# Performance work log

Measured on AMD Instinct MI355X. Metric: run time of the kernel, lower is better.

The kernel has to match this reference:

```python
import jax, jax.numpy as jnp
import numpy as np

D = 200; H = 4; DH = D // H
N_ETYPE = 38; N_NTYPE = 4
B = 256; L = 1024; E = B * L
NODES_PER_G = 200; N = B * NODES_PER_G


def _bn(x, g, b):
    # BatchNorm1d in training mode: batch stats over rows (biased variance, eps=1e-5)
    m = x.mean(axis=0)
    v = x.var(axis=0)
    return (x - m) * jax.lax.rsqrt(v + 1e-5) * g + b


def setup_inputs():
    key = jax.random.key(0)
    ks = jax.random.split(key, 24)
    f = lambda k, s: jax.random.normal(k, s, jnp.float32) * 0.02
    head = jax.random.randint(ks[0], (E,), 0, N)
    tail = (head + 1 + jax.random.randint(ks[1], (E,), 0, N - 1)) % N  # guaranteed no self-loops
    return {
        "x": jax.random.normal(ks[2], (N, D), jnp.float32),
        "node_feature_extra": jax.random.normal(ks[3], (N, D), jnp.float32),
        "sent_vec_r": jax.random.normal(ks[4], (B, D), jnp.float32),
        "We1": f(ks[5], (N_ETYPE + 1 + 2 * N_NTYPE, D)), "be1": jnp.zeros((D,), jnp.float32),
        "ge1": jnp.ones((D,), jnp.float32), "bte1": jnp.zeros((D,), jnp.float32),
        "We2": f(ks[6], (D, D)), "be2": jnp.zeros((D,), jnp.float32),
        "Wa1": f(ks[7], (2 * D, D)), "ba1": jnp.zeros((D,), jnp.float32),
        "ga1": jnp.ones((D,), jnp.float32), "bta1": jnp.zeros((D,), jnp.float32),
        "Wa2": f(ks[8], (D, D)), "ba2": jnp.zeros((D,), jnp.float32),
        "Watt": f(ks[9], (D, D)),
        "Wk": f(ks[10], (2 * D, D)), "bk": jnp.zeros((D,), jnp.float32),
        "Wm": f(ks[11], (2 * D, D)), "bm": jnp.zeros((D,), jnp.float32),
        "Wq": f(ks[12], (D, D)), "bq": jnp.zeros((D,), jnp.float32),
        "Wo1": f(ks[13], (D, D)), "bo1": jnp.zeros((D,), jnp.float32),
        "go1": jnp.ones((D,), jnp.float32), "bto1": jnp.zeros((D,), jnp.float32),
        "Wo2": f(ks[14], (D, D)), "bo2": jnp.zeros((D,), jnp.float32),
        "edge_index": jnp.stack([head, tail]),
        "edge_type": jax.random.randint(ks[15], (E,), 0, N_ETYPE),
        "node_type": jax.random.randint(ks[16], (N,), 0, N_NTYPE),
        "edges_per_graph": L,
    }


def reference(x, node_feature_extra, sent_vec_r, We1, be1, ge1, bte1, We2, be2,
              Wa1, ba1, ga1, bta1, Wa2, ba2, Watt, Wk, bk, Wm, bm, Wq, bq,
              Wo1, bo1, go1, bto1, Wo2, bo2,
              edge_index, edge_type, node_type, edges_per_graph):
    E_, N_ = edge_index.shape[1], x.shape[0]
    src, dst = edge_index[0], edge_index[1]
    x_head, x_tail = x[src], x[dst]
    x_fact = x_tail - x_head
    nt = N_ETYPE + 1
    # original does this segment-mean on detached CPU numpy -> no gradient path
    xf = jax.lax.stop_gradient(x_fact)
    sums = jax.ops.segment_sum(xf, edge_type, num_segments=nt)
    cnts = jax.ops.segment_sum(jnp.ones((E_,), x.dtype), edge_type, num_segments=nt)
    result = (sums / jnp.maximum(cnts, 1.0)[:, None])[edge_type]  # [E, D]
    # one-hot edge/node-type features for real edges + self edges
    edge_vec = jax.nn.one_hot(edge_type, nt, dtype=x.dtype)
    self_edge_vec = jnp.zeros((N_, nt), x.dtype).at[:, N_ETYPE].set(1.0)
    ht = jnp.concatenate([jax.nn.one_hot(node_type[src], N_NTYPE, dtype=x.dtype),
                          jax.nn.one_hot(node_type[dst], N_NTYPE, dtype=x.dtype)], 1)
    sh = jax.nn.one_hot(node_type, N_NTYPE, dtype=x.dtype)
    feat = jnp.concatenate([jnp.concatenate([edge_vec, ht], 1),
                            jnp.concatenate([self_edge_vec, sh, sh], 1)], 0)  # [E+N, 47]
    emb = jax.nn.relu(_bn(feat @ We1 + be1, ge1, bte1)) @ We2 + be2  # edge_encoder, [E+N, D]
    emb_e, emb_self = emb[:E_], emb[E_:]
    # edge_encoder_again on cat([emb_e, result]); split matmul avoids the [E,2D] concat
    h2 = _bn(emb_e @ Wa1[:D] + result @ Wa1[D:] + ba1, ga1, bta1)
    R = jax.nn.relu(h2) @ Wa2 + ba2  # [E, D]
    # per-graph attention: Q rows within a graph are identical (repeated sent_vec),
    # so the LxL softmax has identical rows -> compute one row per graph and broadcast.
    Bg = E_ // edges_per_graph
    Rg = R.reshape(Bg, edges_per_graph, D)
    q = sent_vec_r @ Watt  # [B, D]
    scores = jnp.einsum('bd,bld->bl', q, Rg) / jnp.sqrt(jnp.asarray(D, x.dtype))
    attn = jax.nn.softmax(scores, axis=1)
    upd = jnp.einsum('bl,bld->bd', attn, Rg)
    updated_R = jnp.broadcast_to(upd[:, None, :], Rg.shape).reshape(E_, D)
    edge_attr = jnp.concatenate([updated_R, emb_self], 0)
    # append self-loops (input edge_index has none, matching remove_self_loops)
    loop = jnp.arange(N_, dtype=src.dtype)
    src_all = jnp.concatenate([src, loop])
    dst_all = jnp.concatenate([dst, loop])
    x_i, x_j = x[dst_all], x[src_all]
    key_ = (x_i @ Wk[:D] + edge_attr @ Wk[D:] + bk).reshape(-1, H, DH)
    msg = (x_j @ Wm[:D] + edge_attr @ Wm[D:] + bm).reshape(-1, H, DH)
    qry = ((x_j @ Wq + bq) / jnp.sqrt(jnp.asarray(DH, x.dtype))).reshape(-1, H, DH)
    sc = (qry * key_).sum(-1)  # [E+N, H]
    # segment softmax grouped by source node (every segment non-empty due to self-loops)
    smax = jax.ops.segment_max(sc, src_all, num_segments=N_)
    ex = jnp.exp(sc - smax[src_all])
    den = jax.ops.segment_sum(ex, src_all, num_segments=N_)
    alpha = ex / den[src_all]
    cnt = jax.ops.segment_sum(jnp.ones((src_all.shape[0],), x.dtype), src_all, num_segments=N_)
    alpha = alpha * cnt[src_all][:, None]
    m = (msg * alpha[:, :, None]).reshape(-1, D)
    aggr = jax.ops.segment_sum(m, dst_all, num_segments=N_)  # scatter-add at targets
    return jax.nn.relu(_bn(aggr @ Wo1 + bo1, go1, bto1)) @ Wo2 + bo2
```

## Files before the change

kernel.cpp:

```cpp
#include <hip/hip_runtime.h>

#define D     200
#define H     4
#define DH    50
#define NE    38
#define NTY   4
#define NC    608
#define NCT   612
#define BG    256
#define LG    1024
#define EE    262144
#define NN    51200
#define EA    313344
#define NB    200

#define NTILES 13
#define KSTEPS 7
#define NMATS  8
#define SLICE_SHORTS 13312
#define NCHUNK 26
#define MROWS  128

typedef __attribute__((ext_vector_type(4))) float  f32x4;
typedef __attribute__((ext_vector_type(8))) short  bf16x8;

__device__ __forceinline__ short bf_hi(float f) {
    unsigned u = __float_as_uint(f);
    unsigned r = u + 0x7fffu + ((u >> 16) & 1u);
    return (short)(r >> 16);
}
__device__ __forceinline__ float bf_f(short s) {
    return __uint_as_float(((unsigned)(unsigned short)s) << 16);
}

__global__ __launch_bounds__(256) void k_hist(const int* __restrict__ ei, const int* __restrict__ et,
                                              const int* __restrict__ nt, int* outdeg, int* indeg,
                                              int* __restrict__ hcnt, float* coef) {
    __shared__ int loc[NC];
    int g = blockIdx.x, t = threadIdx.x;
    for (int i = t; i < NC; i += 256) loc[i] = 0;
    __syncthreads();
    #pragma unroll
    for (int j = 0; j < 4; j++) {
        int e = g * LG + j * 256 + t;
        int s = ei[e], d = ei[EE + e], tp = et[e];
        int c = tp * 16 + nt[s] * 4 + nt[d];
        atomicAdd(&loc[c], 1);
        atomicAdd(&outdeg[s], 1);
        atomicAdd(&indeg[d], 1);
        unsafeAtomicAdd(&coef[(size_t)d * NE + tp],  1.f);
        unsafeAtomicAdd(&coef[(size_t)s * NE + tp], -1.f);
    }
    __syncthreads();
    for (int i = t; i < NC; i += 256) hcnt[g * NC + i] = loc[i];
}

__global__ __launch_bounds__(256) void k_hist2(const int* __restrict__ hcnt, int* __restrict__ hist) {
    int c = blockIdx.x * 256 + threadIdx.x;
    if (c >= NC) return;
    int s = 0;
    for (int g = 0; g < BG; g++) s += hcnt[g * NC + c];
    hist[c] = s;
}

__global__ __launch_bounds__(256) void k_ntcnt(const int* __restrict__ nt, int* ntcnt) {
    __shared__ int loc[NTY];
    int t = threadIdx.x;
    if (t < NTY) loc[t] = 0;
    __syncthreads();
    int n = blockIdx.x * 256 + t;
    if (n < NN) atomicAdd(&loc[nt[n]], 1);
    __syncthreads();
    if (t < NTY) atomicAdd(&ntcnt[t], loc[t]);
}

__global__ void k_tcnt(const int* __restrict__ hist, int* tcnt) {
    int t = threadIdx.x;
// ... 206 lines not shown
                s1b += q1 * r[NC + t + 512];
                s1c += q2 * r[2*NC + t + 512];
                s1d += q3 * r[3*NC + t + 512];
            }
        }
        w[t] = (s0a + s0b) + (s0c + s0d);
        if (t < NC - 512) w[t + 512] = (s1a + s1b) + (s1c + s1d);
    }
    __syncthreads();
    float mx = -1e30f;
    for (int c = t; c < NC; c += 512) mx = fmaxf(mx, w[c]);
    for (int o = 32; o; o >>= 1) mx = fmaxf(mx, __shfl_xor(mx, o));
    if (lane == 0) red[wave] = mx;
    __syncthreads();
    mx = red[0];
    #pragma unroll
    for (int i = 1; i < 8; i++) mx = fmaxf(mx, red[i]);
    float sm = 0.f;
    for (int c = t; c < NC; c += 512) {
        float wv = (float)hcnt[b * NC + c] * __expf(w[c] - mx);
        w[c] = wv;
        sm += wv;
    }
    for (int o = 32; o; o >>= 1) sm += __shfl_xor(sm, o);
    if (lane == 0) red[8 + wave] = sm;
    __syncthreads();
    float tot = red[8];
    #pragma unroll
    for (int i = 1; i < 8; i++) tot += red[8 + i];
    float inv = 1.f / tot;
    float a4[4] = {0.f, 0.f, 0.f, 0.f};
    for (int c = wave * (NC/8); c < (wave + 1) * (NC/8); c++) {
        float wv = w[c];
        const float* r = Rc + c * D;
        #pragma unroll
        for (int j = 0; j < 4; j++) { int dd = lane + 64*j; if (dd < D) a4[j] += wv * r[dd]; }
    }
    #pragma unroll
    for (int j = 0; j < 4; j++) { int dd = lane + 64*j; if (dd < D) part[wave][dd] = a4[j]; }
    __syncthreads();
    if (t < D) {
        float s = part[0][t];
        #pragma unroll
        for (int i = 1; i < 8; i++) s += part[i][t];
        upd[b*D + t] = s * inv;
    }
}

__global__ __launch_bounds__(256) void k_packW(const float* __restrict__ Wk, const float* __restrict__ Wm,
                                               const float* __restrict__ Wq, const float* __restrict__ Wo1,
                                               const float* __restrict__ Wo2, const float* __restrict__ Watt,
                                               short* __restrict__ Bpk) {
    int blk = blockIdx.x;
    int mat = blk / (NTILES * KSTEPS);
    int rem = blk - mat * (NTILES * KSTEPS);
    int ks = rem / NTILES, nt = rem - ks * NTILES;
    const float* W = (mat == 0) ? Wk : (mat == 1) ? Wm : (mat == 2) ? Wq : (mat == 3) ? Wo1 :
                     (mat == 4) ? Wo2 : (mat == 5) ? Watt : (mat == 6) ? (Wk + D*D) : (Wm + D*D);
    int t = threadIdx.x;
    for (int idx = t; idx < 1024; idx += 256) {
        int split = idx >> 9;
        int lane = (idx & 511) >> 3;
        int j = idx & 7;
        int n = nt * 16 + (lane & 15);
        int k = ks * 32 + ((lane >> 4) << 3) + j;
        float v = (k < D && n < D) ? W[k * D + n] : 0.f;
        short h = bf_hi(v);
        short out = split ? bf_hi(v - bf_f(h)) : h;
        Bpk[(size_t)blk * 1024 + idx] = out;
    }
}

__device__ __forceinline__ void stage_load8(const short* __restrict__ g, int w, int lane, f32x4 rg[4]) {
    #pragma unroll
    for (int i = 0; i < 4; i++) {
        int c = w + 8 * i;
        if (c < NCHUNK) rg[i] = *(const f32x4*)((const char*)g + c * 1024 + lane * 16);
    }
}
__device__ __forceinline__ void stage_write8(short* l, int w, int lane, const f32x4 rg[4]) {
    #pragma unroll
    for (int i = 0; i < 4; i++) {
        int c = w + 8 * i;
        if (c < NCHUNK) *(f32x4*)((char*)l + c * 1024 + lane * 16) = rg[i];
    }
}

__device__ __forceinline__ void load_afrag(const float* __restrict__ A, int row, int quad, int ks,
                                           int preop, const float* __restrict__ bnacc, float invCnt,
                                           const float* __restrict__ g, const float* __restrict__ bb,
                                           bf16x8& ah, bf16x8& al) {
    int k0 = ks * 32 + quad * 8;
    float v[8];
    if (k0 < D) {
        const float* src = A + (size_t)row * D + k0;
        float4 p0 = *(const float4*)src;
        float4 p1 = *(const float4*)(src + 4);
        v[0]=p0.x; v[1]=p0.y; v[2]=p0.z; v[3]=p0.w;
        v[4]=p1.x; v[5]=p1.y; v[6]=p1.z; v[7]=p1.w;
        if (preop) {
            float4 m0 = *(const float4*)(bnacc + k0);
            float4 m1 = *(const float4*)(bnacc + k0 + 4);
            float4 q0 = *(const float4*)(bnacc + D + k0);
            float4 q1 = *(const float4*)(bnacc + D + k0 + 4);
            float4 g0 = *(const float4*)(g + k0);
            float4 g1 = *(const float4*)(g + k0 + 4);
            float4 b0 = *(const float4*)(bb + k0);
            float4 b1 = *(const float4*)(bb + k0 + 4);
            float mm[8] = {m0.x,m0.y,m0.z,m0.w,m1.x,m1.y,m1.z,m1.w};
            float qq[8] = {q0.x,q0.y,q0.z,q0.w,q1.x,q1.y,q1.z,q1.w};
            float gg[8] = {g0.x,g0.y,g0.z,g0.w,g1.x,g1.y,g1.z,g1.w};
            float bv[8] = {b0.x,b0.y,b0.z,b0.w,b1.x,b1.y,b1.z,b1.w};
            #pragma unroll
            for (int j = 0; j < 8; j++) {
                float mj = mm[j] * invCnt;
                float var = qq[j] * invCnt - mj * mj;
                float rs = rsqrtf(var + 1e-5f);
                float s = rs * gg[j];
                v[j] = fmaxf(v[j] * s + (bv[j] - mj * s), 0.f);
            }
        }
    } else {
        #pragma unroll
        for (int j = 0; j < 8; j++) v[j] = 0.f;
    }
    #pragma unroll
    for (int j = 0; j < 8; j++) {
        short h = bf_hi(v[j]);
        ah[j] = h;
        al[j] = bf_hi(v[j] - bf_f(h));
    }
}

__device__ __forceinline__ void store_C(f32x4 acc[NTILES], float* __restrict__ C, int n0, int w, int lane,
                                        const float* __restrict__ bias, float postscale) {
    int colb = lane & 15, quad = lane >> 4;
    #pragma unroll
    for (int nt = 0; nt < NTILES; nt++) {
        int col = nt * 16 + colb;
        if (col < D) {
            float bj = bias ? bias[col] : 0.f;
            #pragma unroll
            for (int r = 0; r < 4; r++) {
                int row = n0 + w * 16 + quad * 4 + r;
                C[(size_t)row * D + col] = (acc[nt][r] + bj) * postscale;
            }
        }
    }
}

#define MMF_KS(MATV, KS, AH, AL, NUTOT, BASE)                                   \
    {                                                                           \
        int u_ = (MATV) * KSTEPS + (KS);                                        \
        int cur_ = u_ & 1;                                                      \
        if (u_ + 1 < (NUTOT))                                                   \
            stage_load8((BASE) + (size_t)(u_ + 1) * SLICE_SHORTS, w, lane, rg); \
        const bf16x8* B8_ = (const bf16x8*)(Bls + cur_ * SLICE_SHORTS);         \
        _Pragma("unroll")                                                       \
        for (int nt = 0; nt < NTILES; nt++) {                                   \
            bf16x8 bh = B8_[nt * 128 + lane];                                   \
            bf16x8 bl = B8_[nt * 128 + 64 + lane];                              \
            acc[nt] = __builtin_amdgcn_mfma_f32_16x16x32_bf16(AL, bh, acc[nt], 0, 0, 0); \
            acc[nt] = __builtin_amdgcn_mfma_f32_16x16x32_bf16(AH, bl, acc[nt], 0, 0, 0); \
            acc[nt] = __builtin_amdgcn_mfma_f32_16x16x32_bf16(AH, bh, acc[nt], 0, 0, 0); \
        }                                                                       \
        if (u_ + 1 < (NUTOT)) {                                                 \
            stage_write8(Bls + (cur_ ^ 1) * SLICE_SHORTS, w, lane, rg);         \
            __syncthreads();                                                    \
        }                                                                       \
    }

__global__ __launch_bounds__(512, 2) void k_mmf3(const float* __restrict__ A, const short* __restrict__ Bpk,
                                                 const float* __restrict__ bq,
                                                 float* __restrict__ XK, float* __restrict__ XM, float* __restrict__ XQ) {
    __shared__ __align__(16) short Bls[2 * SLICE_SHORTS];
    int t = threadIdx.x, w = t >> 6, lane = t & 63;
    int n0 = blockIdx.x * MROWS;
    int row = n0 + w * 16 + (lane & 15);
    int quad = lane >> 4;
    bf16x8 ah0, al0, ah1, al1, ah2, al2, ah3, al3, ah4, al4, ah5, al5, ah6, al6;
    load_afrag(A, row, quad, 0, 0, nullptr, 0.f, nullptr, nullptr, ah0, al0);
    load_afrag(A, row, quad, 1, 0, nullptr, 0.f, nullptr, nullptr, ah1, al1);
    load_afrag(A, row, quad, 2, 0, nullptr, 0.f, nullptr, nullptr, ah2, al2);
    load_afrag(A, row, quad, 3, 0, nullptr, 0.f, nullptr, nullptr, ah3, al3);
    load_afrag(A, row, quad, 4, 0, nullptr, 0.f, nullptr, nullptr, ah4, al4);
    load_afrag(A, row, quad, 5, 0, nullptr, 0.f, nullptr, nullptr, ah5, al5);
    load_afrag(A, row, quad, 6, 0, nullptr, 0.f, nullptr, nullptr, ah6, al6);
    f32x4 rg[4];
    stage_load8(Bpk, w, lane, rg);
    stage_write8(Bls, w, lane, rg);
    __syncthreads();
    f32x4 acc[NTILES];
    for (int mat = 0; mat < 3; ++mat) {
        #pragma unroll
        for (int nt = 0; nt < NTILES; nt++) { acc[nt][0]=0.f; acc[nt][1]=0.f; acc[nt][2]=0.f; acc[nt][3]=0.f; }
        MMF_KS(mat, 0, ah0, al0, 3*KSTEPS, Bpk)
        MMF_KS(mat, 1, ah1, al1, 3*KSTEPS, Bpk)
        MMF_KS(mat, 2, ah2, al2, 3*KSTEPS, Bpk)
        MMF_KS(mat, 3, ah3, al3, 3*KSTEPS, Bpk)
        MMF_KS(mat, 4, ah4, al4, 3*KSTEPS, Bpk)
        MMF_KS(mat, 5, ah5, al5, 3*KSTEPS, Bpk)
        MMF_KS(mat, 6, ah6, al6, 3*KSTEPS, Bpk)
        if (mat == 0)      store_C(acc, XK, n0, w, lane, nullptr, 1.f);
        else if (mat == 1) store_C(acc, XM, n0, w, lane, nullptr, 1.f);
        else               store_C(acc, XQ, n0, w, lane, bq, 0.14142135623730950488f);
    }
}

__global__ __launch_bounds__(512, 2) void k_mmf(const float* __restrict__ A, const short* __restrict__ Bmat,
                                                const float* __restrict__ bias, float* __restrict__ C,
                                                int preop, const float* __restrict__ bnacc, float invCnt,
                                                const float* __restrict__ g, const float* __restrict__ bb,
                                                float postscale) {
    __shared__ __align__(16) short Bls[2 * SLICE_SHORTS];
    int t = threadIdx.x, w = t >> 6, lane = t & 63;
    int n0 = blockIdx.x * MROWS;
    int row = n0 + w * 16 + (lane & 15);
    int quad = lane >> 4;
    bf16x8 ah0, al0, ah1, al1, ah2, al2, ah3, al3, ah4, al4, ah5, al5, ah6, al6;
    load_afrag(A, row, quad, 0, preop, bnacc, invCnt, g, bb, ah0, al0);
    load_afrag(A, row, quad, 1, preop, bnacc, invCnt, g, bb, ah1, al1);
    load_afrag(A, row, quad, 2, preop, bnacc, invCnt, g, bb, ah2, al2);
    load_afrag(A, row, quad, 3, preop, bnacc, invCnt, g, bb, ah3, al3);
    load_afrag(A, row, quad, 4, preop, bnacc, invCnt, g, bb, ah4, al4);
    load_afrag(A, row, quad, 5, preop, bnacc, invCnt, g, bb, ah5, al5);
    load_afrag(A, row, quad, 6, preop, bnacc, invCnt, g, bb, ah6, al6);
    f32x4 rg[4];
    stage_load8(Bmat, w, lane, rg);
    stage_write8(Bls, w, lane, rg);
    __syncthreads();
    f32x4 acc[NTILES];
    #pragma unroll
    for (int nt = 0; nt < NTILES; nt++) { acc[nt][0]=0.f; acc[nt][1]=0.f; acc[nt][2]=0.f; acc[nt][3]=0.f; }
    MMF_KS(0, 0, ah0, al0, KSTEPS, Bmat)
    MMF_KS(0, 1, ah1, al1, KSTEPS, Bmat)
    MMF_KS(0, 2, ah2, al2, KSTEPS, Bmat)
    MMF_KS(0, 3, ah3, al3, KSTEPS, Bmat)
    MMF_KS(0, 4, ah4, al4, KSTEPS, Bmat)
    MMF_KS(0, 5, ah5, al5, KSTEPS, Bmat)
    MMF_KS(0, 6, ah6, al6, KSTEPS, Bmat)
    store_C(acc, C, n0, w, lane, bias, postscale);
}

__device__ __forceinline__ float head_reduce(float h0, float h1, float h2, float h3, int lane) {
    float ax = (lane < 32) ? h2 : h0;
    float ay = (lane < 32) ? h3 : h1;
    float u0 = ((lane < 32) ? h0 : h2) + __shfl_xor(ax, 32);
    float u1 = ((lane < 32) ? h1 : h3) + __shfl_xor(ay, 32);
    float bx = ((lane & 16) == 0) ? u1 : u0;
    float v  = (((lane & 16) == 0) ? u0 : u1) + __shfl_xor(bx, 16);
    v += __shfl_xor(v, 8);
    v += __shfl_xor(v, 4);
    v += __shfl_xor(v, 2);
    v += __shfl_xor(v, 1);
    return v;
}

__global__ __launch_bounds__(256) void k_soft(const int* __restrict__ ei, const int* __restrict__ nt,
                                              const int* __restrict__ soff, const int* __restrict__ slist,
                                              const int* __restrict__ outdeg,
                                              const float* __restrict__ XQ, const float* __restrict__ XK,
                                              const float* __restrict__ GK, const float* __restrict__ SK,
                                              float* __restrict__ sc, float* __restrict__ scale) {
    int wave = threadIdx.x >> 6, lane = threadIdx.x & 63;
    int n = blockIdx.x * 4 + wave;
    if (n >= NN) return;
    bool act = lane < DH;
    int grp = lane >> 4;
    float qv0 = 0.f, qv1 = 0.f, qv2 = 0.f, qv3 = 0.f;
    if (act) {
        const float* q = XQ + (size_t)n * D + lane;
        qv0 = q[0]; qv1 = q[DH]; qv2 = q[2*DH]; qv3 = q[3*DH];
    }
    float den = 0.f;
    {
        int tn = nt[n];
        float h0 = 0.f, h1 = 0.f, h2 = 0.f, h3 = 0.f;
        if (act) {
            const float* xk = XK + (size_t)n * D + lane;
            const float* sk = SK + (size_t)tn * D + lane;
            h0 = qv0 * (xk[0]    + sk[0]);
            h1 = qv1 * (xk[DH]   + sk[DH]);
            h2 = qv2 * (xk[2*DH] + sk[2*DH]);
            h3 = qv3 * (xk[3*DH] + sk[3*DH]);
        }
        float v = head_reduce(h0, h1, h2, h3, lane);
        float e = __expf(v);
        den += e;
        if ((lane & 15) == 0) sc[(size_t)(EE + n) * 4 + grp] = e;
    }
    int beg = soff[n], end = soff[n + 1];
    for (int i = beg; i < end; i++) {
        int e_ = slist[i];
        int tail = ei[EE + e_];
// ... 88 lines not shown
    const float* bte1 = (const float*)d_in[6];
    const float* We2  = (const float*)d_in[7];
    const float* be2  = (const float*)d_in[8];
    const float* Wa1  = (const float*)d_in[9];
    const float* ba1  = (const float*)d_in[10];
    const float* ga1  = (const float*)d_in[11];
    const float* bta1 = (const float*)d_in[12];
    const float* Wa2  = (const float*)d_in[13];
    const float* ba2  = (const float*)d_in[14];
    const float* Watt = (const float*)d_in[15];
    const float* Wk   = (const float*)d_in[16];
    const float* bk   = (const float*)d_in[17];
    const float* Wm   = (const float*)d_in[18];
    const float* bm   = (const float*)d_in[19];
    const float* Wq   = (const float*)d_in[20];
    const float* bq   = (const float*)d_in[21];
    const float* Wo1  = (const float*)d_in[22];
    const float* bo1  = (const float*)d_in[23];
    const float* go1  = (const float*)d_in[24];
    const float* bto1 = (const float*)d_in[25];
    const float* Wo2  = (const float*)d_in[26];
    const float* bo2  = (const float*)d_in[27];
    const int* ei = (const int*)d_in[28];
    const int* et = (const int*)d_in[29];
    const int* nt = (const int*)d_in[30];

    char* ws = (char*)d_ws;
    size_t off = 0;
    auto alloc = [&](size_t bytes) -> char* {
        char* p = ws + off;
        off = (off + bytes + 255) & ~(size_t)255;
        return p;
    };
    int*   hist   = (int*)  alloc(NC * 4);
    int*   ntcnt  = (int*)  alloc(NTY * 4);
    float* bn1    = (float*)alloc(2 * D * 4);
    float* bn2    = (float*)alloc(2 * D * 4);
    float* bn3    = (float*)alloc(2 * D * 4);
    float* sumsxf = (float*)alloc(NE * D * 4);
    int*   outdeg = (int*)  alloc(NN * 4);
    int*   indeg  = (int*)  alloc(NN * 4);
    int*   hcnt   = (int*)  alloc((size_t)BG * NC * 4);
    float* updS   = (float*)alloc((size_t)384 * D * 4);
    size_t zero_end = off;
    int* tcnt = (int*)alloc(NE * 4);
    int* soff_ = (int*)alloc((NN + 1) * 4);
    int* doff_ = (int*)alloc((NN + 1) * 4);
    int* scur = (int*)alloc(NN * 4);
    int* dcur = (int*)alloc(NN * 4);
    int* bsA  = (int*)alloc(NB * 4);
    int* bsB  = (int*)alloc(NB * 4);
    int* slist = (int*)alloc((size_t)EE * 4);
    int* dlist = (int*)alloc((size_t)EE * 4);
    short* Bpk  = (short*)alloc((size_t)NMATS * NTILES * KSTEPS * 1024 * 2);
    float* h1v   = (float*)alloc((size_t)NCT * D * 4);
    float* embE  = (float*)alloc((size_t)NC * D * 4);
    float* h2pre = (float*)alloc((size_t)NC * D * 4);
    float* Rc    = (float*)alloc((size_t)NC * D * 4);
    float* RcT   = (float*)alloc((size_t)D * NC * 4);
    float* qs    = (float*)alloc((size_t)BG * D * 4);
    float* GK    = (float*)alloc((size_t)384 * D * 4);
    float* GM    = (float*)alloc((size_t)384 * D * 4);
    float* sc    = (float*)alloc((size_t)EA * H * 4);
    float* XK    = (float*)alloc((size_t)NN * D * 4);
    float* XM    = (float*)alloc((size_t)NN * D * 4);
    float* XQ    = (float*)alloc((size_t)NN * D * 4);
    float* coef  = XK;
    float* scale = h1v;
    float* aggr  = XQ;
    float* T1    = XK;
    float* embS  = updS + 256 * D;
    float* SK    = GK + 256 * D;
    float* SM    = GM + 256 * D;

    const int matstride = NTILES * KSTEPS * 1024;

    hipMemsetAsync(ws, 0, zero_end, stream);
    hipMemsetAsync(coef, 0, (size_t)NN * NE * 4, stream);

    k_packW  <<<NMATS * NTILES * KSTEPS, 256, 0, stream>>>(Wk, Wm, Wq, Wo1, Wo2, Watt, Bpk);
    k_hist   <<<BG, 256, 0, stream>>>(ei, et, nt, outdeg, indeg, hcnt, coef);
    k_hist2  <<<3, 256, 0, stream>>>(hcnt, hist);
    k_ntcnt  <<<NN / 256, 256, 0, stream>>>(nt, ntcnt);
    k_tcnt   <<<1, 64, 0, stream>>>(hist, tcnt);
    k_scan_a <<<NB, 256, 0, stream>>>(outdeg, indeg, bsA, bsB);
    k_scan_b <<<1, 256, 0, stream>>>(bsA, bsB, soff_, doff_);
    k_scan_c <<<NB, 256, 0, stream>>>(outdeg, indeg, bsA, bsB, soff_, doff_, scur, dcur);
    k_scatter<<<EE / 256, 256, 0, stream>>>(ei, scur, dcur, slist, dlist);
    k_xfsum3 <<<256, 256, 0, stream>>>(x, coef, sumsxf);
    k_mmf    <<<BG / MROWS, 512, 0, stream>>>(sent, Bpk + (size_t)5 * matstride, nullptr, qs,
                                              0, nullptr, 0.f, nullptr, nullptr, 0.07071067811865475f);
    k_combos1<<<NCT, 256, 0, stream>>>(We1, be1, hist, ntcnt, h1v, bn1);
    k_combos2<<<NCT, 256, 0, stream>>>(h1v, bn1, ge1, bte1, We2, be2, embE, embS);
    k_combos3<<<NC, 256, 0, stream>>>(embE, sumsxf, tcnt, Wa1, ba1, hist, h2pre, bn2);
    k_combos4<<<NC, 256, 0, stream>>>(h2pre, bn2, ga1, bta1, Wa2, ba2, Rc, RcT);
    k_attn   <<<BG, 512, 0, stream>>>(qs, Rc, RcT, hcnt, updS);
    k_mmf    <<<3, 512, 0, stream>>>(updS, Bpk + (size_t)6 * matstride, bk, GK,
                                     0, nullptr, 0.f, nullptr, nullptr, 1.f);
    k_mmf    <<<3, 512, 0, stream>>>(updS, Bpk + (size_t)7 * matstride, bm, GM,
                                     0, nullptr, 0.f, nullptr, nullptr, 1.f);
    k_mmf3   <<<NN / MROWS, 512, 0, stream>>>(x, Bpk, bq, XK, XM, XQ);
    k_soft   <<<NN / 4, 256, 0, stream>>>(ei, nt, soff_, slist, outdeg, XQ, XK, GK, SK, sc, scale);
    k_aggr   <<<NN / 4, 256, 0, stream>>>(ei, nt, doff_, dlist, sc, scale, XM, GM, SM, aggr);
    k_mmf    <<<NN / MROWS, 512, 0, stream>>>(aggr, Bpk + (size_t)3 * matstride, bo1, T1,
                                              0, nullptr, 0.f, nullptr, nullptr, 1.f);
    k_colstats<<<NN / 256, 256, 0, stream>>>(T1, bn3);
    k_mmf    <<<NN / MROWS, 512, 0, stream>>>(T1, Bpk + (size_t)4 * matstride, bo2, (float*)d_out,
                                              1, bn3, 1.f / (float)NN, go1, bto1, 1.f);
}
```

Before: 850.7 us.

## Compute two row tiles per wave in GEMM kernels with four-wave blocks

The MFMA GEMM kernels now run 4 waves per block instead of 8, and each wave computes 32 rows (two 16-row tiles) with two accumulator sets. Each B fragment read from LDS is therefore reused across two A tiles, halving LDS B traffic per MFMA. A fragments are now loaded inside each k-step rather than preloaded for all k-steps, and each thread stages 7 chunks instead of 4. This raises accumulator register pressure, reduces the number of waves per block available to hide latency, and puts global A loads on the critical path of each k-step.

```diff
diff --git a/kernel.cpp b/kernel.cpp
--- a/kernel.cpp
+++ b/kernel.cpp
@@ -354,17 +354,17 @@
     }
 }
 
-__device__ __forceinline__ void stage_load8(const short* __restrict__ g, int w, int lane, f32x4 rg[4]) {
-    #pragma unroll
-    for (int i = 0; i < 4; i++) {
-        int c = w + 8 * i;
+__device__ __forceinline__ void stage_load(const short* __restrict__ g, int w, int lane, f32x4 rg[7]) {
+    #pragma unroll
+    for (int i = 0; i < 7; i++) {
+        int c = w + 4 * i;
         if (c < NCHUNK) rg[i] = *(const f32x4*)((const char*)g + c * 1024 + lane * 16);
     }
 }
-__device__ __forceinline__ void stage_write8(short* l, int w, int lane, const f32x4 rg[4]) {
-    #pragma unroll
-    for (int i = 0; i < 4; i++) {
-        int c = w + 8 * i;
+__device__ __forceinline__ void stage_write(short* l, int w, int lane, const f32x4 rg[7]) {
+    #pragma unroll
+    for (int i = 0; i < 7; i++) {
+        int c = w + 4 * i;
         if (c < NCHUNK) *(f32x4*)((char*)l + c * 1024 + lane * 16) = rg[i];
     }
 }
@@ -415,9 +415,11 @@
     }
 }
 
-__device__ __forceinline__ void store_C(f32x4 acc[NTILES], float* __restrict__ C, int n0, int w, int lane,
-                                        const float* __restrict__ bias, float postscale) {
+__device__ __forceinline__ void store_C2(f32x4 acc0[NTILES], f32x4 acc1[NTILES], float* __restrict__ C,
+                                         int n0, int w, int lane,
+                                         const float* __restrict__ bias, float postscale) {
     int colb = lane & 15, quad = lane >> 4;
+    int rbase = n0 + w * 32;
     #pragma unroll
     for (int nt = 0; nt < NTILES; nt++) {
         int col = nt * 16 + colb;
@@ -425,72 +427,77 @@
             float bj = bias ? bias[col] : 0.f;
             #pragma unroll
             for (int r = 0; r < 4; r++) {
-                int row = n0 + w * 16 + quad * 4 + r;
-                C[(size_t)row * D + col] = (acc[nt][r] + bj) * postscale;
+                int row = rbase + quad * 4 + r;
+                C[(size_t)row * D + col]        = (acc0[nt][r] + bj) * postscale;
+                C[(size_t)(row + 16) * D + col] = (acc1[nt][r] + bj) * postscale;
             }
         }
     }
 }
 
-#define MMF_KS(MATV, KS, AH, AL, NUTOT, BASE)                                   \
+#define MMF_KS(MATV, KS, NUTOT, BASE)                                           \
     {                                                                           \
         int u_ = (MATV) * KSTEPS + (KS);                                        \
         int cur_ = u_ & 1;                                                      \
         if (u_ + 1 < (NUTOT))                                                   \
-            stage_load8((BASE) + (size_t)(u_ + 1) * SLICE_SHORTS, w, lane, rg); \
+            stage_load((BASE) + (size_t)(u_ + 1) * SLICE_SHORTS, w, lane, rg);  \
+        bf16x8 ah0_, al0_, ah1_, al1_;                                          \
+        load_afrag(A, row0, quad, KS, preop_, bnacc_, invCnt_, g_, bb_, ah0_, al0_); \
+        load_afrag(A, row1, quad, KS, preop_, bnacc_, invCnt_, g_, bb_, ah1_, al1_); \
         const bf16x8* B8_ = (const bf16x8*)(Bls + cur_ * SLICE_SHORTS);         \
         _Pragma("unroll")                                                       \
         for (int nt = 0; nt < NTILES; nt++) {                                   \
             bf16x8 bh = B8_[nt * 128 + lane];                                   \
             bf16x8 bl = B8_[nt * 128 + 64 + lane];                              \
-            acc[nt] = __builtin_amdgcn_mfma_f32_16x16x32_bf16(AL, bh, acc[nt], 0, 0, 0); \
-            acc[nt] = __builtin_amdgcn_mfma_f32_16x16x32_bf16(AH, bl, acc[nt], 0, 0, 0); \
-            acc[nt] = __builtin_amdgcn_mfma_f32_16x16x32_bf16(AH, bh, acc[nt], 0, 0, 0); \
+            acc0[nt] = __builtin_amdgcn_mfma_f32_16x16x32_bf16(al0_, bh, acc0[nt], 0, 0, 0); \
+            acc0[nt] = __builtin_amdgcn_mfma_f32_16x16x32_bf16(ah0_, bl, acc0[nt], 0, 0, 0); \
+            acc0[nt] = __builtin_amdgcn_mfma_f32_16x16x32_bf16(ah0_, bh, acc0[nt], 0, 0, 0); \
+            acc1[nt] = __builtin_amdgcn_mfma_f32_16x16x32_bf16(al1_, bh, acc1[nt], 0, 0, 0); \
+            acc1[nt] = __builtin_amdgcn_mfma_f32_16x16x32_bf16(ah1_, bl, acc1[nt], 0, 0, 0); \
+            acc1[nt] = __builtin_amdgcn_mfma_f32_16x16x32_bf16(ah1_, bh, acc1[nt], 0, 0, 0); \
         }                                                                       \
         if (u_ + 1 < (NUTOT)) {                                                 \
-            stage_write8(Bls + (cur_ ^ 1) * SLICE_SHORTS, w, lane, rg);         \
+            stage_write(Bls + (cur_ ^ 1) * SLICE_SHORTS, w, lane, rg);          \
             __syncthreads();                                                    \
         }                                                                       \
     }
 
-__global__ __launch_bounds__(512, 2) void k_mmf3(const float* __restrict__ A, const short* __restrict__ Bpk,
+__global__ __launch_bounds__(256, 2) void k_mmf3(const float* __restrict__ A, const short* __restrict__ Bpk,
                                                  const float* __restrict__ bq,
                                                  float* __restrict__ XK, float* __restrict__ XM, float* __restrict__ XQ) {
     __shared__ __align__(16) short Bls[2 * SLICE_SHORTS];
     int t = threadIdx.x, w = t >> 6, lane = t & 63;
     int n0 = blockIdx.x * MROWS;
-    int row = n0 + w * 16 + (lane & 15);
+    int row0 = n0 + w * 32 + (lane & 15);
+    int row1 = row0 + 16;
     int quad = lane >> 4;
-    bf16x8 ah0, al0, ah1, al1, ah2, al2, ah3, al3, ah4, al4, ah5, al5, ah6, al6;
-    load_afrag(A, row, quad, 0, 0, nullptr, 0.f, nullptr, nullptr, ah0, al0);
-    load_afrag(A, row, quad, 1, 0, nullptr, 0.f, nullptr, nullptr, ah1, al1);
-    load_afrag(A, row, quad, 2, 0, nullptr, 0.f, nullptr, nullptr, ah2, al2);
-    load_afrag(A, row, quad, 3, 0, nullptr, 0.f, nullptr, nullptr, ah3, al3);
-    load_afrag(A, row, quad, 4, 0, nullptr, 0.f, nullptr, nullptr, ah4, al4);
-    load_afrag(A, row, quad, 5, 0, nullptr, 0.f, nullptr, nullptr, ah5, al5);
-    load_afrag(A, row, quad, 6, 0, nullptr, 0.f, nullptr, nullptr, ah6, al6);
-    f32x4 rg[4];
-    stage_load8(Bpk, w, lane, rg);
-    stage_write8(Bls, w, lane, rg);
-    __syncthreads();
-    f32x4 acc[NTILES];
+    int preop_ = 0; const float* bnacc_ = nullptr; float invCnt_ = 0.f;
+    const float* g_ = nullptr; const float* bb_ = nullptr;
+    f32x4 rg[7];
+    stage_load(Bpk, w, lane, rg);
+    stage_write(Bls, w, lane, rg);
+    __syncthreads();
+    f32x4 acc0[NTILES], acc1[NTILES];
     for (int mat = 0; mat < 3; ++mat) {
         #pragma unroll
-        for (int nt = 0; nt < NTILES; nt++) { acc[nt][0]=0.f; acc[nt][1]=0.f; acc[nt][2]=0.f; acc[nt][3]=0.f; }
-        MMF_KS(mat, 0, ah0, al0, 3*KSTEPS, Bpk)
-        MMF_KS(mat, 1, ah1, al1, 3*KSTEPS, Bpk)
-        MMF_KS(mat, 2, ah2, al2, 3*KSTEPS, Bpk)
-        MMF_KS(mat, 3, ah3, al3, 3*KSTEPS, Bpk)
-        MMF_KS(mat, 4, ah4, al4, 3*KSTEPS, Bpk)
-        MMF_KS(mat, 5, ah5, al5, 3*KSTEPS, Bpk)
-        MMF_KS(mat, 6, ah6, al6, 3*KSTEPS, Bpk)
-        if (mat == 0)      store_C(acc, XK, n0, w, lane, nullptr, 1.f);
-        else if (mat == 1) store_C(acc, XM, n0, w, lane, nullptr, 1.f);
-        else               store_C(acc, XQ, n0, w, lane, bq, 0.14142135623730950488f);
-    }
-}
-
-__global__ __launch_bounds__(512, 2) void k_mmf(const float* __restrict__ A, const short* __restrict__ Bmat,
+        for (int nt = 0; nt < NTILES; nt++) {
+            acc0[nt][0]=0.f; acc0[nt][1]=0.f; acc0[nt][2]=0.f; acc0[nt][3]=0.f;
+            acc1[nt][0]=0.f; acc1[nt][1]=0.f; acc1[nt][2]=0.f; acc1[nt][3]=0.f;
+        }
+        MMF_KS(mat, 0, 3*KSTEPS, Bpk)
+        MMF_KS(mat, 1, 3*KSTEPS, Bpk)
+        MMF_KS(mat, 2, 3*KSTEPS, Bpk)
+        MMF_KS(mat, 3, 3*KSTEPS, Bpk)
+        MMF_KS(mat, 4, 3*KSTEPS, Bpk)
+        MMF_KS(mat, 5, 3*KSTEPS, Bpk)
+        MMF_KS(mat, 6, 3*KSTEPS, Bpk)
+        if (mat == 0)      store_C2(acc0, acc1, XK, n0, w, lane, nullptr, 1.f);
+        else if (mat == 1) store_C2(acc0, acc1, XM, n0, w, lane, nullptr, 1.f);
+        else               store_C2(acc0, acc1, XQ, n0, w, lane, bq, 0.14142135623730950488f);
+    }
+}
+
+__global__ __launch_bounds__(256, 2) void k_mmf(const float* __restrict__ A, const short* __restrict__ Bmat,
                                                 const float* __restrict__ bias, float* __restrict__ C,
                                                 int preop, const float* __restrict__ bnacc, float invCnt,
                                                 const float* __restrict__ g, const float* __restrict__ bb,
@@ -498,31 +505,29 @@
     __shared__ __align__(16) short Bls[2 * SLICE_SHORTS];
     int t = threadIdx.x, w = t >> 6, lane = t & 63;
     int n0 = blockIdx.x * MROWS;
-    int row = n0 + w * 16 + (lane & 15);
+    int row0 = n0 + w * 32 + (lane & 15);
+    int row1 = row0 + 16;
     int quad = lane >> 4;
-    bf16x8 ah0, al0, ah1, al1, ah2, al2, ah3, al3, ah4, al4, ah5, al5, ah6, al6;
-    load_afrag(A, row, quad, 0, preop, bnacc, invCnt, g, bb, ah0, al0);
-    load_afrag(A, row, quad, 1, preop, bnacc, invCnt, g, bb, ah1, al1);
-    load_afrag(A, row, quad, 2, preop, bnacc, invCnt, g, bb, ah2, al2);
-    load_afrag(A, row, quad, 3, preop, bnacc, invCnt, g, bb, ah3, al3);
-    load_afrag(A, row, quad, 4, preop, bnacc, invCnt, g, bb, ah4, al4);
-    load_afrag(A, row, quad, 5, preop, bnacc, invCnt, g, bb, ah5, al5);
-    load_afrag(A, row, quad, 6, preop, bnacc, invCnt, g, bb, ah6, al6);
-    f32x4 rg[4];
-    stage_load8(Bmat, w, lane, rg);
-    stage_write8(Bls, w, lane, rg);
-    __syncthreads();
-    f32x4 acc[NTILES];
-    #pragma unroll
-    for (int nt = 0; nt < NTILES; nt++) { acc[nt][0]=0.f; acc[nt][1]=0.f; acc[nt][2]=0.f; acc[nt][3]=0.f; }
-    MMF_KS(0, 0, ah0, al0, KSTEPS, Bmat)
-    MMF_KS(0, 1, ah1, al1, KSTEPS, Bmat)
-    MMF_KS(0, 2, ah2, al2, KSTEPS, Bmat)
-    MMF_KS(0, 3, ah3, al3, KSTEPS, Bmat)
-    MMF_KS(0, 4, ah4, al4, KSTEPS, Bmat)
-    MMF_KS(0, 5, ah5, al5, KSTEPS, Bmat)
-    MMF_KS(0, 6, ah6, al6, KSTEPS, Bmat)
-    store_C(acc, C, n0, w, lane, bias, postscale);
+    int preop_ = preop; const float* bnacc_ = bnacc; float invCnt_ = invCnt;
+    const float* g_ = g; const float* bb_ = bb;
+    f32x4 rg[7];
+    stage_load(Bmat, w, lane, rg);
+    stage_write(Bls, w, lane, rg);
+    __syncthreads();
+    f32x4 acc0[NTILES], acc1[NTILES];
+    #pragma unroll
+    for (int nt = 0; nt < NTILES; nt++) {
+        acc0[nt][0]=0.f; acc0[nt][1]=0.f; acc0[nt][2]=0.f; acc0[nt][3]=0.f;
+        acc1[nt][0]=0.f; acc1[nt][1]=0.f; acc1[nt][2]=0.f; acc1[nt][3]=0.f;
+    }
+    MMF_KS(0, 0, KSTEPS, Bmat)
+    MMF_KS(0, 1, KSTEPS, Bmat)
+    MMF_KS(0, 2, KSTEPS, Bmat)
+    MMF_KS(0, 3, KSTEPS, Bmat)
+    MMF_KS(0, 4, KSTEPS, Bmat)
+    MMF_KS(0, 5, KSTEPS, Bmat)
+    MMF_KS(0, 6, KSTEPS, Bmat)
+    store_C2(acc0, acc1, C, n0, w, lane, bias, postscale);
 }
 
 __device__ __forceinline__ float head_reduce(float h0, float h1, float h2, float h3, int lane) {
@@ -753,23 +758,23 @@
     k_scan_c <<<NB, 256, 0, stream>>>(outdeg, indeg, bsA, bsB, soff_, doff_, scur, dcur);
     k_scatter<<<EE / 256, 256, 0, stream>>>(ei, scur, dcur, slist, dlist);
     k_xfsum3 <<<256, 256, 0, stream>>>(x, coef, sumsxf);
-    k_mmf    <<<BG / MROWS, 512, 0, stream>>>(sent, Bpk + (size_t)5 * matstride, nullptr, qs,
+    k_mmf    <<<BG / MROWS, 256, 0, stream>>>(sent, Bpk + (size_t)5 * matstride, nullptr, qs,
                                               0, nullptr, 0.f, nullptr, nullptr, 0.07071067811865475f);
     k_combos1<<<NCT, 256, 0, stream>>>(We1, be1, hist, ntcnt, h1v, bn1);
     k_combos2<<<NCT, 256, 0, stream>>>(h1v, bn1, ge1, bte1, We2, be2, embE, embS);
     k_combos3<<<NC, 256, 0, stream>>>(embE, sumsxf, tcnt, Wa1, ba1, hist, h2pre, bn2);
     k_combos4<<<NC, 256, 0, stream>>>(h2pre, bn2, ga1, bta1, Wa2, ba2, Rc, RcT);
     k_attn   <<<BG, 512, 0, stream>>>(qs, Rc, RcT, hcnt, updS);
-    k_mmf    <<<3, 512, 0, stream>>>(updS, Bpk + (size_t)6 * matstride, bk, GK,
+    k_mmf    <<<3, 256, 0, stream>>>(updS, Bpk + (size_t)6 * matstride, bk, GK,
                                      0, nullptr, 0.f, nullptr, nullptr, 1.f);
-    k_mmf    <<<3, 512, 0, stream>>>(updS, Bpk + (size_t)7 * matstride, bm, GM,
+    k_mmf    <<<3, 256, 0, stream>>>(updS, Bpk + (size_t)7 * matstride, bm, GM,
                                      0, nullptr, 0.f, nullptr, nullptr, 1.f);
-    k_mmf3   <<<NN / MROWS, 512, 0, stream>>>(x, Bpk, bq, XK, XM, XQ);
+    k_mmf3   <<<NN / MROWS, 256, 0, stream>>>(x, Bpk, bq, XK, XM, XQ);
     k_soft   <<<NN / 4, 256, 0, stream>>>(ei, nt, soff_, slist, outdeg, XQ, XK, GK, SK, sc, scale);
     k_aggr   <<<NN / 4, 256, 0, stream>>>(ei, nt, doff_, dlist, sc, scale, XM, GM, SM, aggr);
-    k_mmf    <<<NN / MROWS, 512, 0, stream>>>(aggr, Bpk + (size_t)3 * matstride, bo1, T1,
+    k_mmf    <<<NN / MROWS, 256, 0, stream>>>(aggr, Bpk + (size_t)3 * matstride, bo1, T1,
                                               0, nullptr, 0.f, nullptr, nullptr, 1.f);
     k_colstats<<<NN / 256, 256, 0, stream>>>(T1, bn3);
-    k_mmf    <<<NN / MROWS, 512, 0, stream>>>(T1, Bpk + (size_t)4 * matstride, bo2, (float*)d_out,
+    k_mmf    <<<NN / MROWS, 256, 0, stream>>>(T1, Bpk + (size_t)4 * matstride, bo2, (float*)d_out,
                                               1, bn3, 1.f / (float)NN, go1, bto1, 1.f);
 }
```

Measured after the change: 1.010 ms. 1.19x slower.

## Switch dense GEMMs to 32x32x16 MFMA tiles with per-kstep A loads

Applied to the files above, without the earlier changes.

Rewrites the split-bf16 (hi/lo) GEMM kernels to use 32x32x16 MFMA instructions. Each wave now covers a 32-row by 128-column output block, where before it covered 16 rows across all 13 column tiles. The weight packing is redone for 16-wide k slices of 256 columns, and A fragments are loaded per k-step instead of all up front. This is meant to cut register pressure and LDS traffic per flop, at the cost of more k-steps and more barriers. The padded column range (256 vs 208) adds some wasted MFMA work.

```diff
diff --git a/kernel.cpp b/kernel.cpp
--- a/kernel.cpp
+++ b/kernel.cpp
@@ -14,15 +14,14 @@
 #define EA    313344
 #define NB    200
 
-#define NTILES 13
-#define KSTEPS 7
 #define NMATS  8
-#define SLICE_SHORTS 13312
-#define NCHUNK 26
 #define MROWS  128
-
-typedef __attribute__((ext_vector_type(4))) float  f32x4;
-typedef __attribute__((ext_vector_type(8))) short  bf16x8;
+#define KS16   13
+#define SL32_SHORTS 8192
+
+typedef __attribute__((ext_vector_type(4)))  float f32x4;
+typedef __attribute__((ext_vector_type(16))) float f32x16;
+typedef __attribute__((ext_vector_type(8)))  short bf16x8;
 
 __device__ __forceinline__ short bf_hi(float f) {
     unsigned u = __float_as_uint(f);
@@ -335,45 +334,38 @@
                                                const float* __restrict__ Wo2, const float* __restrict__ Watt,
                                                short* __restrict__ Bpk) {
     int blk = blockIdx.x;
-    int mat = blk / (NTILES * KSTEPS);
-    int rem = blk - mat * (NTILES * KSTEPS);
-    int ks = rem / NTILES, nt = rem - ks * NTILES;
+    int mat = blk / KS16, ks = blk - mat * KS16;
     const float* W = (mat == 0) ? Wk : (mat == 1) ? Wm : (mat == 2) ? Wq : (mat == 3) ? Wo1 :
                      (mat == 4) ? Wo2 : (mat == 5) ? Watt : (mat == 6) ? (Wk + D*D) : (Wm + D*D);
     int t = threadIdx.x;
-    for (int idx = t; idx < 1024; idx += 256) {
-        int split = idx >> 9;
-        int lane = (idx & 511) >> 3;
-        int j = idx & 7;
-        int n = nt * 16 + (lane & 15);
-        int k = ks * 32 + ((lane >> 4) << 3) + j;
+    for (int idx = t; idx < SL32_SHORTS; idx += 256) {
+        int frag = idx >> 9;
+        int within = idx & 511;
+        int tile = frag >> 1, half = frag & 1;
+        int lane = within >> 3, j = within & 7;
+        int n = tile * 32 + (lane & 31);
+        int k = ks * 16 + ((lane >> 5) << 3) + j;
         float v = (k < D && n < D) ? W[k * D + n] : 0.f;
         short h = bf_hi(v);
-        short out = split ? bf_hi(v - bf_f(h)) : h;
-        Bpk[(size_t)blk * 1024 + idx] = out;
-    }
-}
-
-__device__ __forceinline__ void stage_load8(const short* __restrict__ g, int w, int lane, f32x4 rg[4]) {
-    #pragma unroll
-    for (int i = 0; i < 4; i++) {
-        int c = w + 8 * i;
-        if (c < NCHUNK) rg[i] = *(const f32x4*)((const char*)g + c * 1024 + lane * 16);
-    }
-}
-__device__ __forceinline__ void stage_write8(short* l, int w, int lane, const f32x4 rg[4]) {
-    #pragma unroll
-    for (int i = 0; i < 4; i++) {
-        int c = w + 8 * i;
-        if (c < NCHUNK) *(f32x4*)((char*)l + c * 1024 + lane * 16) = rg[i];
-    }
-}
-
-__device__ __forceinline__ void load_afrag(const float* __restrict__ A, int row, int quad, int ks,
-                                           int preop, const float* __restrict__ bnacc, float invCnt,
-                                           const float* __restrict__ g, const float* __restrict__ bb,
-                                           bf16x8& ah, bf16x8& al) {
-    int k0 = ks * 32 + quad * 8;
+        short out = half ? bf_hi(v - bf_f(h)) : h;
+        Bpk[(size_t)blk * SL32_SHORTS + idx] = out;
+    }
+}
+
+__device__ __forceinline__ void stage_load32(const short* __restrict__ g, int w, int lane, f32x4 rg[2]) {
+    rg[0] = *(const f32x4*)((const char*)g + w * 1024 + lane * 16);
+    rg[1] = *(const f32x4*)((const char*)g + (w + 8) * 1024 + lane * 16);
+}
+__device__ __forceinline__ void stage_write32(short* l, int w, int lane, const f32x4 rg[2]) {
+    *(f32x4*)((char*)l + w * 1024 + lane * 16) = rg[0];
+    *(f32x4*)((char*)l + (w + 8) * 1024 + lane * 16) = rg[1];
+}
+
+__device__ __forceinline__ void load_afrag32(const float* __restrict__ A, int row, int khalf, int ks,
+                                             int preop, const float* __restrict__ bnacc, float invCnt,
+                                             const float* __restrict__ g, const float* __restrict__ bb,
+                                             bf16x8& ah, bf16x8& al) {
+    int k0 = ks * 16 + khalf * 8;
     float v[8];
     if (k0 < D) {
         const float* src = A + (size_t)row * D + k0;
@@ -415,78 +407,92 @@
     }
 }
 
-__device__ __forceinline__ void store_C(f32x4 acc[NTILES], float* __restrict__ C, int n0, int w, int lane,
-                                        const float* __restrict__ bias, float postscale) {
-    int colb = lane & 15, quad = lane >> 4;
-    #pragma unroll
-    for (int nt = 0; nt < NTILES; nt++) {
-        int col = nt * 16 + colb;
-        if (col < D) {
-            float bj = bias ? bias[col] : 0.f;
-            #pragma unroll
-            for (int r = 0; r < 4; r++) {
-                int row = n0 + w * 16 + quad * 4 + r;
-                C[(size_t)row * D + col] = (acc[nt][r] + bj) * postscale;
-            }
+__device__ __forceinline__ void store_C32(const f32x16& a, float* __restrict__ C, int n0, int rowg,
+                                          int tg, int lane, const float* __restrict__ bias, float postscale) {
+    int col = tg * 32 + (lane & 31);
+    if (col < D) {
+        float bj = bias ? bias[col] : 0.f;
+        int rbase = n0 + rowg * 32 + 4 * (lane >> 5);
+        #pragma unroll
+        for (int r = 0; r < 16; r++) {
+            int row = rbase + (r & 3) + 8 * (r >> 2);
+            C[(size_t)row * D + col] = (a[r] + bj) * postscale;
         }
     }
 }
 
-#define MMF_KS(MATV, KS, AH, AL, NUTOT, BASE)                                   \
-    {                                                                           \
-        int u_ = (MATV) * KSTEPS + (KS);                                        \
-        int cur_ = u_ & 1;                                                      \
-        if (u_ + 1 < (NUTOT))                                                   \
-            stage_load8((BASE) + (size_t)(u_ + 1) * SLICE_SHORTS, w, lane, rg); \
-        const bf16x8* B8_ = (const bf16x8*)(Bls + cur_ * SLICE_SHORTS);         \
-        _Pragma("unroll")                                                       \
-        for (int nt = 0; nt < NTILES; nt++) {                                   \
-            bf16x8 bh = B8_[nt * 128 + lane];                                   \
-            bf16x8 bl = B8_[nt * 128 + 64 + lane];                              \
-            acc[nt] = __builtin_amdgcn_mfma_f32_16x16x32_bf16(AL, bh, acc[nt], 0, 0, 0); \
-            acc[nt] = __builtin_amdgcn_mfma_f32_16x16x32_bf16(AH, bl, acc[nt], 0, 0, 0); \
-            acc[nt] = __builtin_amdgcn_mfma_f32_16x16x32_bf16(AH, bh, acc[nt], 0, 0, 0); \
-        }                                                                       \
-        if (u_ + 1 < (NUTOT)) {                                                 \
-            stage_write8(Bls + (cur_ ^ 1) * SLICE_SHORTS, w, lane, rg);         \
-            __syncthreads();                                                    \
-        }                                                                       \
-    }
+#define MMF32_KS(MATV, KS, NUTOT, BASE)                                           \
+    {                                                                             \
+        int u_ = (MATV) * KS16 + (KS);                                            \
+        int cur_ = u_ & 1;                                                        \
+        if (u_ + 1 < (NUTOT))                                                     \
+            stage_load32((BASE) + (size_t)(u_ + 1) * SL32_SHORTS, w, lane, rg);   \
+        bf16x8 ah_, al_;                                                          \
+        load_afrag32(A, row, khalf, KS, preop_, bnacc_, invCnt_, g_, bb_, ah_, al_); \
+        const bf16x8* B8_ = (const bf16x8*)(Bls + cur_ * SL32_SHORTS);            \
+        { bf16x8 bh = B8_[((tb+0)*2+0)*64 + lane], bl = B8_[((tb+0)*2+1)*64 + lane]; \
+          acc0 = __builtin_amdgcn_mfma_f32_32x32x16_bf16(al_, bh, acc0, 0, 0, 0); \
+          acc0 = __builtin_amdgcn_mfma_f32_32x32x16_bf16(ah_, bl, acc0, 0, 0, 0); \
+          acc0 = __builtin_amdgcn_mfma_f32_32x32x16_bf16(ah_, bh, acc0, 0, 0, 0); } \
+        { bf16x8 bh = B8_[((tb+1)*2+0)*64 + lane], bl = B8_[((tb+1)*2+1)*64 + lane]; \
+          acc1 = __builtin_amdgcn_mfma_f32_32x32x16_bf16(al_, bh, acc1, 0, 0, 0); \
+          acc1 = __builtin_amdgcn_mfma_f32_32x32x16_bf16(ah_, bl, acc1, 0, 0, 0); \
+          acc1 = __builtin_amdgcn_mfma_f32_32x32x16_bf16(ah_, bh, acc1, 0, 0, 0); } \
+        { bf16x8 bh = B8_[((tb+2)*2+0)*64 + lane], bl = B8_[((tb+2)*2+1)*64 + lane]; \
+          acc2 = __builtin_amdgcn_mfma_f32_32x32x16_bf16(al_, bh, acc2, 0, 0, 0); \
+          acc2 = __builtin_amdgcn_mfma_f32_32x32x16_bf16(ah_, bl, acc2, 0, 0, 0); \
+          acc2 = __builtin_amdgcn_mfma_f32_32x32x16_bf16(ah_, bh, acc2, 0, 0, 0); } \
+        { bf16x8 bh = B8_[((tb+3)*2+0)*64 + lane], bl = B8_[((tb+3)*2+1)*64 + lane]; \
+          acc3 = __builtin_amdgcn_mfma_f32_32x32x16_bf16(al_, bh, acc3, 0, 0, 0); \
+          acc3 = __builtin_amdgcn_mfma_f32_32x32x16_bf16(ah_, bl, acc3, 0, 0, 0); \
+          acc3 = __builtin_amdgcn_mfma_f32_32x32x16_bf16(ah_, bh, acc3, 0, 0, 0); } \
+        if (u_ + 1 < (NUTOT)) {                                                   \
+            stage_write32(Bls + (cur_ ^ 1) * SL32_SHORTS, w, lane, rg);           \
+            __syncthreads();                                                      \
+        }                                                                         \
+    }
+
+#define ZERO_ACCS() { _Pragma("unroll") for (int r_ = 0; r_ < 16; r_++) { acc0[r_]=0.f; acc1[r_]=0.f; acc2[r_]=0.f; acc3[r_]=0.f; } }
 
 __global__ __launch_bounds__(512, 2) void k_mmf3(const float* __restrict__ A, const short* __restrict__ Bpk,
                                                  const float* __restrict__ bq,
                                                  float* __restrict__ XK, float* __restrict__ XM, float* __restrict__ XQ) {
-    __shared__ __align__(16) short Bls[2 * SLICE_SHORTS];
+    __shared__ __align__(16) short Bls[2 * SL32_SHORTS];
     int t = threadIdx.x, w = t >> 6, lane = t & 63;
     int n0 = blockIdx.x * MROWS;
-    int row = n0 + w * 16 + (lane & 15);
-    int quad = lane >> 4;
-    bf16x8 ah0, al0, ah1, al1, ah2, al2, ah3, al3, ah4, al4, ah5, al5, ah6, al6;
-    load_afrag(A, row, quad, 0, 0, nullptr, 0.f, nullptr, nullptr, ah0, al0);
-    load_afrag(A, row, quad, 1, 0, nullptr, 0.f, nullptr, nullptr, ah1, al1);
-    load_afrag(A, row, quad, 2, 0, nullptr, 0.f, nullptr, nullptr, ah2, al2);
-    load_afrag(A, row, quad, 3, 0, nullptr, 0.f, nullptr, nullptr, ah3, al3);
-    load_afrag(A, row, quad, 4, 0, nullptr, 0.f, nullptr, nullptr, ah4, al4);
-    load_afrag(A, row, quad, 5, 0, nullptr, 0.f, nullptr, nullptr, ah5, al5);
-    load_afrag(A, row, quad, 6, 0, nullptr, 0.f, nullptr, nullptr, ah6, al6);
-    f32x4 rg[4];
-    stage_load8(Bpk, w, lane, rg);
-    stage_write8(Bls, w, lane, rg);
-    __syncthreads();
-    f32x4 acc[NTILES];
+    int rowg = w >> 1, colg = w & 1;
+    int tb = colg * 4;
+    int row = n0 + rowg * 32 + (lane & 31);
+    int khalf = lane >> 5;
+    int preop_ = 0; const float* bnacc_ = nullptr; float invCnt_ = 0.f;
+    const float* g_ = nullptr; const float* bb_ = nullptr;
+    f32x4 rg[2];
+    stage_load32(Bpk, w, lane, rg);
+    stage_write32(Bls, w, lane, rg);
+    __syncthreads();
+    f32x16 acc0, acc1, acc2, acc3;
     for (int mat = 0; mat < 3; ++mat) {
-        #pragma unroll
-        for (int nt = 0; nt < NTILES; nt++) { acc[nt][0]=0.f; acc[nt][1]=0.f; acc[nt][2]=0.f; acc[nt][3]=0.f; }
-        MMF_KS(mat, 0, ah0, al0, 3*KSTEPS, Bpk)
-        MMF_KS(mat, 1, ah1, al1, 3*KSTEPS, Bpk)
-        MMF_KS(mat, 2, ah2, al2, 3*KSTEPS, Bpk)
-        MMF_KS(mat, 3, ah3, al3, 3*KSTEPS, Bpk)
-        MMF_KS(mat, 4, ah4, al4, 3*KSTEPS, Bpk)
-        MMF_KS(mat, 5, ah5, al5, 3*KSTEPS, Bpk)
-        MMF_KS(mat, 6, ah6, al6, 3*KSTEPS, Bpk)
-        if (mat == 0)      store_C(acc, XK, n0, w, lane, nullptr, 1.f);
-        else if (mat == 1) store_C(acc, XM, n0, w, lane, nullptr, 1.f);
-        else               store_C(acc, XQ, n0, w, lane, bq, 0.14142135623730950488f);
+        ZERO_ACCS()
+        MMF32_KS(mat,  0, 3*KS16, Bpk)
+        MMF32_KS(mat,  1, 3*KS16, Bpk)
+        MMF32_KS(mat,  2, 3*KS16, Bpk)
+        MMF32_KS(mat,  3, 3*KS16, Bpk)
+        MMF32_KS(mat,  4, 3*KS16, Bpk)
+        MMF32_KS(mat,  5, 3*KS16, Bpk)
+        MMF32_KS(mat,  6, 3*KS16, Bpk)
+        MMF32_KS(mat,  7, 3*KS16, Bpk)
+        MMF32_KS(mat,  8, 3*KS16, Bpk)
+        MMF32_KS(mat,  9, 3*KS16, Bpk)
+        MMF32_KS(mat, 10, 3*KS16, Bpk)
+        MMF32_KS(mat, 11, 3*KS16, Bpk)
+        MMF32_KS(mat, 12, 3*KS16, Bpk)
+        float* C = (mat == 0) ? XK : (mat == 1) ? XM : XQ;
+        const float* bias = (mat == 2) ? bq : nullptr;
+        float ps = (mat == 2) ? 0.14142135623730950488f : 1.f;
+        store_C32(acc0, C, n0, rowg, tb + 0, lane, bias, ps);
+        store_C32(acc1, C, n0, rowg, tb + 1, lane, bias, ps);
+        store_C32(acc2, C, n0, rowg, tb + 2, lane, bias, ps);
+        store_C32(acc3, C, n0, rowg, tb + 3, lane, bias, ps);
     }
 }
 
@@ -495,34 +501,38 @@
                                                 int preop, const float* __restrict__ bnacc, float invCnt,
                                                 const float* __restrict__ g, const float* __restrict__ bb,
                                                 float postscale) {
-    __shared__ __align__(16) short Bls[2 * SLICE_SHORTS];
+    __shared__ __align__(16) short Bls[2 * SL32_SHORTS];
     int t = threadIdx.x, w = t >> 6, lane = t & 63;
     int n0 = blockIdx.x * MROWS;
-    int row = n0 + w * 16 + (lane & 15);
-    int quad = lane >> 4;
-    bf16x8 ah0, al0, ah1, al1, ah2, al2, ah3, al3, ah4, al4, ah5, al5, ah6, al6;
-    load_afrag(A, row, quad, 0, preop, bnacc, invCnt, g, bb, ah0, al0);
-    load_afrag(A, row, quad, 1, preop, bnacc, invCnt, g, bb, ah1, al1);
-    load_afrag(A, row, quad, 2, preop, bnacc, invCnt, g, bb, ah2, al2);
-    load_afrag(A, row, quad, 3, preop, bnacc, invCnt, g, bb, ah3, al3);
-    load_afrag(A, row, quad, 4, preop, bnacc, invCnt, g, bb, ah4, al4);
-    load_afrag(A, row, quad, 5, preop, bnacc, invCnt, g, bb, ah5, al5);
-    load_afrag(A, row, quad, 6, preop, bnacc, invCnt, g, bb, ah6, al6);
-    f32x4 rg[4];
-    stage_load8(Bmat, w, lane, rg);
-    stage_write8(Bls, w, lane, rg);
-    __syncthreads();
-    f32x4 acc[NTILES];
-    #pragma unroll
-    for (int nt = 0; nt < NTILES; nt++) { acc[nt][0]=0.f; acc[nt][1]=0.f; acc[nt][2]=0.f; acc[nt][3]=0.f; }
-    MMF_KS(0, 0, ah0, al0, KSTEPS, Bmat)
-    MMF_KS(0, 1, ah1, al1, KSTEPS, Bmat)
-    MMF_KS(0, 2, ah2, al2, KSTEPS, Bmat)
-    MMF_KS(0, 3, ah3, al3, KSTEPS, Bmat)
-    MMF_KS(0, 4, ah4, al4, KSTEPS, Bmat)
-    MMF_KS(0, 5, ah5, al5, KSTEPS, Bmat)
-    MMF_KS(0, 6, ah6, al6, KSTEPS, Bmat)
-    store_C(acc, C, n0, w, lane, bias, postscale);
+    int rowg = w >> 1, colg = w & 1;
+    int tb = colg * 4;
+    int row = n0 + rowg * 32 + (lane & 31);
+    int khalf = lane >> 5;
+    int preop_ = preop; const float* bnacc_ = bnacc; float invCnt_ = invCnt;
+    const float* g_ = g; const float* bb_ = bb;
+    f32x4 rg[2];
+    stage_load32(Bmat, w, lane, rg);
+    stage_write32(Bls, w, lane, rg);
+    __syncthreads();
+    f32x16 acc0, acc1, acc2, acc3;
+    ZERO_ACCS()
+    MMF32_KS(0,  0, KS16, Bmat)
+    MMF32_KS(0,  1, KS16, Bmat)
+    MMF32_KS(0,  2, KS16, Bmat)
+    MMF32_KS(0,  3, KS16, Bmat)
+    MMF32_KS(0,  4, KS16, Bmat)
+    MMF32_KS(0,  5, KS16, Bmat)
+    MMF32_KS(0,  6, KS16, Bmat)
+    MMF32_KS(0,  7, KS16, Bmat)
+    MMF32_KS(0,  8, KS16, Bmat)
+    MMF32_KS(0,  9, KS16, Bmat)
+    MMF32_KS(0, 10, KS16, Bmat)
+    MMF32_KS(0, 11, KS16, Bmat)
+    MMF32_KS(0, 12, KS16, Bmat)
+    store_C32(acc0, C, n0, rowg, tb + 0, lane, bias, postscale);
+    store_C32(acc1, C, n0, rowg, tb + 1, lane, bias, postscale);
+    store_C32(acc2, C, n0, rowg, tb + 2, lane, bias, postscale);
+    store_C32(acc3, C, n0, rowg, tb + 3, lane, bias, postscale);
 }
 
 __device__ __forceinline__ float head_reduce(float h0, float h1, float h2, float h3, int lane) {
@@ -717,7 +727,7 @@
     int* bsB  = (int*)alloc(NB * 4);
     int* slist = (int*)alloc((size_t)EE * 4);
     int* dlist = (int*)alloc((size_t)EE * 4);
-    short* Bpk  = (short*)alloc((size_t)NMATS * NTILES * KSTEPS * 1024 * 2);
+    short* Bpk  = (short*)alloc((size_t)NMATS * KS16 * SL32_SHORTS * 2);
     float* h1v   = (float*)alloc((size_t)NCT * D * 4);
     float* embE  = (float*)alloc((size_t)NC * D * 4);
     float* h2pre = (float*)alloc((size_t)NC * D * 4);
@@ -738,12 +748,12 @@
     float* SK    = GK + 256 * D;
     float* SM    = GM + 256 * D;
 
-    const int matstride = NTILES * KSTEPS * 1024;
+    const size_t matstride = (size_t)KS16 * SL32_SHORTS;
 
     hipMemsetAsync(ws, 0, zero_end, stream);
     hipMemsetAsync(coef, 0, (size_t)NN * NE * 4, stream);
 
-    k_packW  <<<NMATS * NTILES * KSTEPS, 256, 0, stream>>>(Wk, Wm, Wq, Wo1, Wo2, Watt, Bpk);
+    k_packW  <<<NMATS * KS16, 256, 0, stream>>>(Wk, Wm, Wq, Wo1, Wo2, Watt, Bpk);
     k_hist   <<<BG, 256, 0, stream>>>(ei, et, nt, outdeg, indeg, hcnt, coef);
     k_hist2  <<<3, 256, 0, stream>>>(hcnt, hist);
     k_ntcnt  <<<NN / 256, 256, 0, stream>>>(nt, ntcnt);
```

Result: slower. 878.3 us (+3.2%).
